# Performance work log

Hardware: AMD Instinct MI355X
Metric: run time of the kernel (lower is better)

## Reference

```python
import jax, jax.numpy as jnp
import numpy as np

B, N, D, NS, ITERS = 64, 4096, 256, 8, 3
EPS_ATTN = 1e-5   # module eps (added to attn)
EPS_LN = 1e-5     # torch LayerNorm default eps


def layer_norm(x, g, b):
    m = jnp.mean(x, axis=-1, keepdims=True)
    v = jnp.mean((x - m) ** 2, axis=-1, keepdims=True)
    return (x - m) / jnp.sqrt(v + EPS_LN) * g + b


def setup_inputs() -> dict:
    key = jax.random.key(0)
    ks = jax.random.split(key, 16)
    s = 0.02
    return {
        "inputs": jax.random.normal(ks[0], (B, N, D), jnp.float32),
        "slots_init": jax.random.normal(ks[1], (1, NS, D), jnp.float32),
        "Wq": jax.random.normal(ks[2], (D, D), jnp.float32) * s,
        "Wk": jax.random.normal(ks[3], (D, D), jnp.float32) * s,
        "Wv": jax.random.normal(ks[4], (D, D), jnp.float32) * s,
        "W_ih": jax.random.normal(ks[5], (3 * D, D), jnp.float32) * s,
        "W_hh": jax.random.normal(ks[6], (3 * D, D), jnp.float32) * s,
        "b_ih": jnp.zeros((3 * D,), jnp.float32),
        "b_hh": jnp.zeros((3 * D,), jnp.float32),
        "ln_in_g": jnp.ones((D,), jnp.float32),
        "ln_in_b": jnp.zeros((D,), jnp.float32),
        "ln_s_g": jnp.ones((D,), jnp.float32),
        "ln_s_b": jnp.zeros((D,), jnp.float32),
        "ln_m_g": jnp.ones((D,), jnp.float32),
        "ln_m_b": jnp.zeros((D,), jnp.float32),
        "W1": jax.random.normal(ks[7], (4 * D, D), jnp.float32) * s,
        "b1": jnp.zeros((4 * D,), jnp.float32),
        "W2": jax.random.normal(ks[8], (D, 4 * D), jnp.float32) * s,
        "b2": jnp.zeros((D,), jnp.float32),
    }


def gru_cell(x, h, W_ih, W_hh, b_ih, b_hh):
    # x, h: [M, D]; PyTorch GRU cell equations (gate order r, z, n)
    gi = x @ W_ih.T + b_ih
    gh = h @ W_hh.T + b_hh
    gi_r, gi_z, gi_n = jnp.split(gi, 3, axis=-1)
    gh_r, gh_z, gh_n = jnp.split(gh, 3, axis=-1)
    r = jax.nn.sigmoid(gi_r + gh_r)
    z = jax.nn.sigmoid(gi_z + gh_z)
    n = jnp.tanh(gi_n + r * gh_n)
    return (1.0 - z) * n + z * h


def reference(inputs, slots_init, Wq, Wk, Wv, W_ih, W_hh, b_ih, b_hh,
              ln_in_g, ln_in_b, ln_s_g, ln_s_b, ln_m_g, ln_m_b,
              W1, b1, W2, b2):
    b, n, d = inputs.shape
    scale = d ** -0.5
    slots = jnp.broadcast_to(slots_init, (b, NS, d))

    x = layer_norm(inputs, ln_in_g, ln_in_b)
    k = x @ Wk.T  # [b, n, d]
    v = x @ Wv.T  # [b, n, d]

    for _ in range(ITERS):
        slots_prev = slots
        s_n = layer_norm(slots, ln_s_g, ln_s_b)
        q = s_n @ Wq.T  # [b, ns, d]
        dots = jnp.einsum('bid,bjd->bij', q, k) * scale  # [b, ns, n]
        attn = jax.nn.softmax(dots, axis=1) + EPS_ATTN   # softmax over slots
        attn = attn / jnp.mean(attn, axis=-1, keepdims=True)
        updates = jnp.einsum('bjd,bij->bid', v, attn)     # [b, ns, d]
        h = gru_cell(updates.reshape(-1, d), slots_prev.reshape(-1, d),
                     W_ih, W_hh, b_ih, b_hh)
        slots = h.reshape(b, NS, d)
        # residual MLP with pre-norm
        y = layer_norm(slots, ln_m_g, ln_m_b)
        y = jax.nn.leaky_relu(y @ W1.T + b1, negative_slope=0.01)
        slots = slots + (y @ W2.T + b2)
    return slots
```

## Files before the change

kernel.cpp:

```cpp
#include <hip/hip_runtime.h>
#include <hip/hip_fp16.h>
#include <hip/hip_bf16.h>


#define BB 64
#define NN 4096
#define DD 256
#define NSL 8
#define NITER 3

__device__ __forceinline__ float wredsum(float v){
#pragma unroll
  for(int m=32;m;m>>=1) v += __shfl_xor(v, m, 64);
  return v;
}
__device__ __forceinline__ float2 u2f2(unsigned u){ __half2 h; __builtin_memcpy(&h,&u,4); return __half22float2(h); }
__device__ __forceinline__ float sigm(float v){ return 1.0f/(1.0f+__expf(-v)); }

union U4 { uint4 u; __half2 h[4]; };

__global__ __launch_bounds__(256) void k_prep(
    const float* __restrict__ Whh, const float* __restrict__ W1,
    const float* __restrict__ W2,  const float* __restrict__ sinit,
    __half* __restrict__ Wg, __half* __restrict__ W1t, __half* __restrict__ W2t,
    float* __restrict__ slots){
  for(int idx=blockIdx.x*256+threadIdx.x; idx<851968; idx+=gridDim.x*256){
    if(idx<196608){ int col=idx>>8, c=idx&255; Wg[(size_t)c*1536+768+col]=__float2half(Whh[idx]); }
    else if(idx<458752){ int k=idx-196608; int col=k>>8, c=k&255; W1t[(size_t)c*1024+col]=__float2half(W1[k]); }
    else if(idx<720896){ int k=idx-458752; int col=k>>10, c=k&1023; W2t[(size_t)c*256+col]=__float2half(W2[k]); }
    else { int k=idx-720896; slots[k]=sinit[k&2047]; }
  }
}

__global__ __launch_bounds__(256) void k_WC(const float* __restrict__ Wih, const float* __restrict__ Wv,
                                            __half* __restrict__ Wg){
  int col=blockIdx.x;
  int t=threadIdx.x;
  __shared__ float wr[256];
  wr[t]=Wih[col*256+t];
  __syncthreads();
  float acc=0.f;
#pragma unroll 8
  for(int d=0;d<256;d++) acc += wr[d]*Wv[d*256+t];
  Wg[(size_t)t*1536+col]=__float2half(acc);
}

__global__ __launch_bounds__(256) void k_M(const float* __restrict__ Wq, const float* __restrict__ Wk,
                                           __half* __restrict__ M2h){
  int c = blockIdx.x, e = threadIdx.x;
  float acc = 0.f;
#pragma unroll 8
  for(int d=0; d<256; d++) acc += Wq[d*256+e]*Wk[d*256+c];
  M2h[c*256+e] = __float2half(acc * 0.0625f);
}

__global__ __launch_bounds__(256) void k_ln_x(const float* __restrict__ in, const float* __restrict__ g,
                                              const float* __restrict__ bbv, __half* __restrict__ x){
  int row  = blockIdx.x*4 + (threadIdx.x>>6);
  int lane = threadIdx.x&63;
  const float4 v = ((const float4*)(in + (size_t)row*DD))[lane];
  float s  = v.x+v.y+v.z+v.w;
  float ss = v.x*v.x+v.y*v.y+v.z*v.z+v.w*v.w;
  s = wredsum(s); ss = wredsum(ss);
  float m = s*(1.0f/256.0f);
  float r = rsqrtf(ss*(1.0f/256.0f) - m*m + 1e-5f);
  float4 gv = ((const float4*)g)[lane];
  float4 bv = ((const float4*)bbv)[lane];
  float y0=(v.x-m)*r*gv.x+bv.x, y1=(v.y-m)*r*gv.y+bv.y;
  float y2=(v.z-m)*r*gv.z+bv.z, y3=(v.w-m)*r*gv.w+bv.w;
  __half2 h0=__floats2half2_rn(y0,y1), h1=__floats2half2_rn(y2,y3);
  uint2 u; __builtin_memcpy(&u.x,&h0,4); __builtin_memcpy(&u.y,&h1,4);
  ((uint2*)(x + (size_t)row*DD))[lane] = u;
}

__global__ __launch_bounds__(256) void k_pre(const float* __restrict__ slots, const float* __restrict__ g,
                                             const float* __restrict__ bbv, const __half* __restrict__ M2h,
                                             float* __restrict__ qs){
  int row = blockIdx.x;
  int t = threadIdx.x;
  __shared__ __align__(16) float sn[256];
  __shared__ float red[8];
  float v = slots[row*256 + t];
  float s = wredsum(v), ss = wredsum(v*v);
  int wid=t>>6, lane=t&63;
  if(lane==0){ red[wid]=s; red[4+wid]=ss; }
  __syncthreads();
  float S  = red[0]+red[1]+red[2]+red[3];
  float SS = red[4]+red[5]+red[6]+red[7];
  float m = S*(1.0f/256.0f);
  float r = rsqrtf(SS*(1.0f/256.0f) - m*m + 1e-5f);
  sn[t] = (v-m)*r*g[t]+bbv[t];
  __syncthreads();
  const uint4* w4 = (const uint4*)(M2h + (size_t)t*256);
  float acc=0.f;
#pragma unroll 4
  for(int kk=0;kk<32;kk++){
    U4 w; w.u=w4[kk];
#pragma unroll
    for(int q=0;q<4;q++){
      float2 f=__half22float2(w.h[q]);
      acc += sn[kk*8+2*q]*f.x + sn[kk*8+2*q+1]*f.y;
    }
  }
  qs[row*256+t]=acc;
}

__global__ __launch_bounds__(256) void k_att(const __half* __restrict__ x, const float* __restrict__ qs,
                                             float* __restrict__ pagg){
  int b = blockIdx.x>>4;
  int t = threadIdx.x;
  size_t j = (size_t)blockIdx.x*256 + t;
  __shared__ __align__(16) float qt[256][8];
  __shared__ __align__(16) float wl[256][8];
  __shared__ __align__(16) float aggl[4][2048];
  __shared__ float wsl[4][8];
  const float* qb = qs + b*2048;
  for(int e=t;e<2048;e+=256) qt[e&255][e>>8]=qb[e];
  __syncthreads();
  const uint4* xr = (const uint4*)(x + j*DD);
  float pd[8]={0,0,0,0,0,0,0,0};
#pragma unroll 2
  for(int ch=0; ch<32; ch++){
    uint4 u = xr[ch];
    float2 f0=u2f2(u.x), f1=u2f2(u.y), f2=u2f2(u.z), f3=u2f2(u.w);
    float xv[8]={f0.x,f0.y,f1.x,f1.y,f2.x,f2.y,f3.x,f3.y};
    int c0=ch*8;
#pragma unroll
    for(int cc=0;cc<8;cc++){
      const float4* qp=(const float4*)&qt[c0+cc][0];
      float4 qa=qp[0], qc=qp[1];
      float xvv=xv[cc];
      pd[0]+=qa.x*xvv; pd[1]+=qa.y*xvv; pd[2]+=qa.z*xvv; pd[3]+=qa.w*xvv;
      pd[4]+=qc.x*xvv; pd[5]+=qc.y*xvv; pd[6]+=qc.z*xvv; pd[7]+=qc.w*xvv;
    }
  }
  float mx=pd[0];
#pragma unroll
  for(int i=1;i<8;i++) mx=fmaxf(mx,pd[i]);
  float ev[8]; float ssum=0.f;
#pragma unroll
  for(int i=0;i<8;i++){ ev[i]=__expf(pd[i]-mx); ssum+=ev[i]; }
  float inv=1.0f/ssum;
#pragma unroll
  for(int i=0;i<8;i++) wl[t][i]=ev[i]*inv+1e-5f;
  __syncthreads();
  int wid=t>>6, lane=t&63;
  float acc[8][4];
#pragma unroll
  for(int i=0;i<8;i++){ acc[i][0]=0;acc[i][1]=0;acc[i][2]=0;acc[i][3]=0; }
  float ws[8]={0,0,0,0,0,0,0,0};
  for(int r=0;r<64;r++){
    int jl = wid*64 + r;
    uint2 u = ((const uint2*)(x + ((size_t)blockIdx.x*256 + jl)*DD))[lane];
    float2 f01=u2f2(u.x), f23=u2f2(u.y);
    const float4* wp=(const float4*)&wl[jl][0];
    float4 wa=wp[0], wb_=wp[1];
    float wv[8]={wa.x,wa.y,wa.z,wa.w,wb_.x,wb_.y,wb_.z,wb_.w};
    float xv[4]={f01.x,f01.y,f23.x,f23.y};
#pragma unroll
    for(int i=0;i<8;i++){
      acc[i][0]+=wv[i]*xv[0]; acc[i][1]+=wv[i]*xv[1];
      acc[i][2]+=wv[i]*xv[2]; acc[i][3]+=wv[i]*xv[3];
      ws[i]+=wv[i];
    }
  }
#pragma unroll
  for(int i=0;i<8;i++){
    float4 st={acc[i][0],acc[i][1],acc[i][2],acc[i][3]};
    *((float4*)&aggl[wid][i*256 + lane*4])=st;
  }
  if(lane==0){
#pragma unroll
    for(int i=0;i<8;i++) wsl[wid][i]=ws[i];
  }
  __syncthreads();
  float* pb = pagg + (size_t)blockIdx.x*2064;
  for(int e=t;e<2048;e+=256) pb[e]=aggl[0][e]+aggl[1][e]+aggl[2][e]+aggl[3][e];
  if(t<8) pb[2048+t]=wsl[0][t]+wsl[1][t]+wsl[2][t]+wsl[3][t];
}

__global__ __launch_bounds__(512) void t_gates2(
    const float* __restrict__ pagg, const float* __restrict__ slots_in,
    const __half* __restrict__ Wg, const float* __restrict__ bih, const float* __restrict__ bhh,
    const float* __restrict__ lm_g, const float* __restrict__ lm_b,
    float* __restrict__ hb, __half* __restrict__ ysh){
  int row0=blockIdx.x*2;
  int b=row0>>3, i0=row0&7;
  int t=threadIdx.x;
  int r=t>>8, c=t&255;
  __shared__ float AS[4][256];
  __shared__ __align__(16) float gl[2][1536];
  __shared__ float fac[2];
  __shared__ float redS[2][4], redQ[2][4];
  const float* pb = pagg + (size_t)b*16*2064;
  {
    float s=0.f;
#pragma unroll
    for(int ch=0;ch<16;ch++) s += pb[ch*2064 + (i0+r)*256 + c];
    AS[r][c]=s;
    AS[2+r][c]=slots_in[(size_t)(row0+r)*256+c];
  }
  if(t<2){
    float s=0.f;
#pragma unroll
    for(int ch=0;ch<16;ch++) s += pb[ch*2064 + 2048 + i0 + t];
    fac[t]=4096.0f/s;
  }
  __syncthreads();
  AS[r][c] *= fac[r];
  __syncthreads();
  if(t<384){
    int c0=t*4;
    bool ih = c0<768;
    const float* X0 = ih? AS[0] : AS[2];
    const float* X1 = ih? AS[1] : AS[3];
    const __half* wb = Wg + c0;
    float a00=0,a01=0,a02=0,a03=0, a10=0,a11=0,a12=0,a13=0;
#pragma unroll 8
    for(int k=0;k<256;k++){
      uint2 u = *(const uint2*)(wb + (size_t)k*1536);
      float2 f0=u2f2(u.x), f1=u2f2(u.y);
      float x0=X0[k], x1=X1[k];
      a00+=x0*f0.x; a01+=x0*f0.y; a02+=x0*f1.x; a03+=x0*f1.y;
      a10+=x1*f0.x; a11+=x1*f0.y; a12+=x1*f1.x; a13+=x1*f1.y;
    }
    const float* bb = ih? bih : bhh;
    int bc = ih? c0 : c0-768;
    float4 bv=*(const float4*)&bb[bc];
    gl[0][c0]=a00+bv.x; gl[0][c0+1]=a01+bv.y; gl[0][c0+2]=a02+bv.z; gl[0][c0+3]=a03+bv.w;
    gl[1][c0]=a10+bv.x; gl[1][c0+1]=a11+bv.y; gl[1][c0+2]=a12+bv.z; gl[1][c0+3]=a13+bv.w;
  }
  __syncthreads();
  {
    float gir=gl[r][c], giz=gl[r][256+c], gin=gl[r][512+c];
    float ghr=gl[r][768+c], ghz=gl[r][1024+c], ghn=gl[r][1280+c];
    float hp=AS[2+r][c];
    float rr=sigm(gir+ghr), z=sigm(giz+ghz);
    float n=tanhf(gin+rr*ghn);
    float hv=(1.0f-z)*n+z*hp;
    hb[(size_t)(row0+r)*256+c]=hv;
    float s=wredsum(hv), ss=wredsum(hv*hv);
    if((t&63)==0){ redS[r][(t>>6)&3]=s; redQ[r][(t>>6)&3]=ss; }
    __syncthreads();
    float S_=redS[r][0]+redS[r][1]+redS[r][2]+redS[r][3];
    float SS=redQ[r][0]+redQ[r][1]+redQ[r][2]+redQ[r][3];
    float m=S_*(1.0f/256.0f);
    float rs=rsqrtf(SS*(1.0f/256.0f)-m*m+1e-5f);
    ysh[(size_t)(row0+r)*256+c]=__float2half((hv-m)*rs*lm_g[c]+lm_b[c]);
  }
}

__global__ __launch_bounds__(512) void t_mlp(
    const float* __restrict__ hb, const __half* __restrict__ ysg,
    const __half* __restrict__ W1t, const float* __restrict__ b1,
    const __half* __restrict__ W2t, const float* __restrict__ b2,
    const float* __restrict__ ls_g, const float* __restrict__ ls_b,
    const __half* __restrict__ M2h,
    float* __restrict__ dst, float* __restrict__ qs, int last){
  int row0=blockIdx.x*2;
  int t=threadIdx.x;
  int r=t>>8, c=t&255;
  __shared__ float ys[2][256];
  __shared__ __align__(16) float pz[2][2][1024];
  __shared__ __align__(16) float z1[2][1024];
  __shared__ float pm[2][4][256];
  __shared__ float redS[2][4], redQ[2][4];
  ys[r][c]=__half2float(ysg[(size_t)(row0+r)*256+c]);
  __syncthreads();
  {
    int c0=c*4;
    const __half* wb = W1t + (size_t)r*128*1024 + c0;
    float a00=0,a01=0,a02=0,a03=0, a10=0,a11=0,a12=0,a13=0;
#pragma unroll 8
    for(int k=0;k<128;k++){
      uint2 u=*(const uint2*)(wb + (size_t)k*1024);
      float2 f0=u2f2(u.x), f1=u2f2(u.y);
      float x0=ys[0][r*128+k], x1=ys[1][r*128+k];
      a00+=x0*f0.x; a01+=x0*f0.y; a02+=x0*f1.x; a03+=x0*f1.y;
      a10+=x1*f0.x; a11+=x1*f0.y; a12+=x1*f1.x; a13+=x1*f1.y;
    }
    pz[r][0][c0]=a00; pz[r][0][c0+1]=a01; pz[r][0][c0+2]=a02; pz[r][0][c0+3]=a03;
    pz[r][1][c0]=a10; pz[r][1][c0+1]=a11; pz[r][1][c0+2]=a12; pz[r][1][c0+3]=a13;
  }
  __syncthreads();
  for(int idx=t; idx<2048; idx+=512){
    int rr2=idx>>10, cc=idx&1023;
    float v=pz[0][rr2][cc]+pz[1][rr2][cc]+b1[cc];
    z1[rr2][cc]= v>0.f? v : 0.01f*v;
  }
  __syncthreads();
  if(t<256){
    int ks4=t>>6, cg=t&63;
    int c0=cg*4;
    const __half* wb = W2t + (size_t)ks4*256*256 + c0;
    float a00=0,a01=0,a02=0,a03=0, a10=0,a11=0,a12=0,a13=0;
#pragma unroll 8
    for(int k=0;k<256;k++){
      uint2 u=*(const uint2*)(wb + (size_t)k*256);
      float2 f0=u2f2(u.x), f1=u2f2(u.y);
      float x0=z1[0][ks4*256+k], x1=z1[1][ks4*256+k];
      a00+=x0*f0.x; a01+=x0*f0.y; a02+=x0*f1.x; a03+=x0*f1.y;
      a10+=x1*f0.x; a11+=x1*f0.y; a12+=x1*f1.x; a13+=x1*f1.y;
    }
    pm[0][ks4][c0]=a00; pm[0][ks4][c0+1]=a01; pm[0][ks4][c0+2]=a02; pm[0][ks4][c0+3]=a03;
    pm[1][ks4][c0]=a10; pm[1][ks4][c0+1]=a11; pm[1][ks4][c0+2]=a12; pm[1][ks4][c0+3]=a13;
  }
  __syncthreads();
  float s = hb[(size_t)(row0+r)*256+c] + pm[r][0][c]+pm[r][1][c]+pm[r][2][c]+pm[r][3][c] + b2[c];
  dst[(size_t)(row0+r)*256+c]=s;
  if(last) return;
  float su=wredsum(s), sq=wredsum(s*s);
  if((t&63)==0){ redS[r][(t>>6)&3]=su; redQ[r][(t>>6)&3]=sq; }
  __syncthreads();
  float S_=redS[r][0]+redS[r][1]+redS[r][2]+redS[r][3];
  float SS=redQ[r][0]+redQ[r][1]+redQ[r][2]+redQ[r][3];
  float m=S_*(1.0f/256.0f);
  float rs=rsqrtf(SS*(1.0f/256.0f)-m*m+1e-5f);
  ys[r][c]=(s-m)*rs*ls_g[c]+ls_b[c];
  __syncthreads();
  {
    const uint4* m4=(const uint4*)(M2h+(size_t)c*256);
    float acc=0.f;
#pragma unroll 4
    for(int kk=0;kk<32;kk++){
      U4 w; w.u=m4[kk];
#pragma unroll
      for(int q=0;q<4;q++){
        float2 f=__half22float2(w.h[q]);
        acc += ys[r][kk*8+2*q]*f.x + ys[r][kk*8+2*q+1]*f.y;
      }
    }
    qs[(size_t)(row0+r)*256+c]=acc;
  }
}

extern "C" void kernel_launch(void* const* d_in, const int* in_sizes, int n_in,
                              void* d_out, int out_size, void* d_ws, size_t ws_size,
                              hipStream_t stream){
  const float* inputs=(const float*)d_in[0];
  const float* sinit =(const float*)d_in[1];
  const float* Wq =(const float*)d_in[2];
  const float* Wk =(const float*)d_in[3];
  const float* Wv =(const float*)d_in[4];
  const float* Wih=(const float*)d_in[5];
  const float* Whh=(const float*)d_in[6];
  const float* bih=(const float*)d_in[7];
  const float* bhh=(const float*)d_in[8];
  const float* lin_g=(const float*)d_in[9];
  const float* lin_b=(const float*)d_in[10];
  const float* ls_g=(const float*)d_in[11];
  const float* ls_b=(const float*)d_in[12];
  const float* lm_g=(const float*)d_in[13];
  const float* lm_b=(const float*)d_in[14];
  const float* W1=(const float*)d_in[15];
  const float* b1=(const float*)d_in[16];
  const float* W2=(const float*)d_in[17];
  const float* b2=(const float*)d_in[18];

  char* w=(char*)d_ws;
  __half* x    =(__half*)w; w += (size_t)BB*NN*DD*2;
  float* qs    =(float*)w;  w += 512*256*4;
  float* slots =(float*)w;  w += 512*256*4;
  float* pagg  =(float*)w;  w += (size_t)1024*2064*4;
  __half* M2h  =(__half*)w; w += 256*256*2;
  __half* Wg   =(__half*)w; w += 256*1536*2;
  __half* W1t  =(__half*)w; w += 256*1024*2;
  __half* W2t  =(__half*)w; w += 1024*256*2;
  float* hb    =(float*)w;  w += 512*256*4;
  __half* ysh  =(__half*)w; w += 512*256*2;

  hipLaunchKernelGGL(k_prep, dim3(1664), dim3(256), 0, stream,
                     Whh, W1, W2, sinit, Wg, W1t, W2t, slots);
  hipLaunchKernelGGL(k_WC,   dim3(768),  dim3(256), 0, stream, Wih, Wv, Wg);
  hipLaunchKernelGGL(k_M,    dim3(256),  dim3(256), 0, stream, Wq, Wk, M2h);
  hipLaunchKernelGGL(k_ln_x, dim3(65536),dim3(256), 0, stream, inputs, lin_g, lin_b, x);
  hipLaunchKernelGGL(k_pre,  dim3(512),  dim3(256), 0, stream, slots, ls_g, ls_b, M2h, qs);
  for(int it=0; it<NITER; ++it){
    int last = (it==NITER-1);
    float* dst = last ? (float*)d_out : slots;
    hipLaunchKernelGGL(k_att,    dim3(1024), dim3(256), 0, stream, x, qs, pagg);
    hipLaunchKernelGGL(t_gates2, dim3(256),  dim3(512), 0, stream, pagg, slots, Wg, bih, bhh,
                       lm_g, lm_b, hb, ysh);
    hipLaunchKernelGGL(t_mlp,    dim3(256),  dim3(512), 0, stream, hb, ysh, W1t, b1, W2t, b2,
                       ls_g, ls_b, M2h, dst, qs, last);
  }
}
```

Before: 462.2 us.

## Tile small-slot GEMMs through LDS, atomically reduce attention partials, merge prep kernels

Merges the three weight-prep kernels into one launch that also zeroes per-iteration accumulation buffers and writes a transposed copy of the Wq·Wk product. The attention kernel now reduces its partial aggregates with global atomics into per-iteration buffers, replacing the 16-way partial-buffer reduction in the gate kernel. The GRU-gate and MLP kernels now process 4 slot rows per block, staging fp16 weight tiles in shared memory, so each weight load is reused across more rows and block count halves. The intermediate post-LayerNorm activations are kept in fp32 instead of fp16. In exchange there are many more __syncthreads, fewer blocks in flight, and atomic contention in k_att.

```diff
diff --git a/kernel.cpp b/kernel.cpp
--- a/kernel.cpp
+++ b/kernel.cpp
@@ -19,39 +19,87 @@
 
 union U4 { uint4 u; __half2 h[4]; };
 
-__global__ __launch_bounds__(256) void k_prep(
+#define TG_STAGE(WSRC, LDW, C0) do{ \
+  _Pragma("unroll") \
+  for(int q=0;q<8;q++){ \
+    int u_=q*512+t; int kk_=u_>>4, cb_=u_&15; \
+    *(uint4*)&Wst[kk_][cb_*8] = *(const uint4*)((WSRC) + (size_t)kk_*(LDW) + (C0) + cb_*8); \
+  } \
+}while(0)
+
+#define TG_COMPUTE(APTR, ASTR) do{ \
+  float acc_[4][4]={{0,0,0,0},{0,0,0,0},{0,0,0,0},{0,0,0,0}}; \
+  _Pragma("unroll") \
+  for(int g_=0;g_<4;g_++){ \
+    int kb_=ks*16+g_*4; \
+    float av_[4][4]; \
+    _Pragma("unroll") \
+    for(int r_=0;r_<4;r_++){ \
+      float4 a_=*(const float4*)((APTR) + r_*(ASTR) + kb_); \
+      av_[r_][0]=a_.x; av_[r_][1]=a_.y; av_[r_][2]=a_.z; av_[r_][3]=a_.w; \
+    } \
+    _Pragma("unroll") \
+    for(int k2_=0;k2_<4;k2_++){ \
+      uint2 wv_=*(const uint2*)&Wst[kb_+k2_][c4*4]; \
+      float2 wa_=u2f2(wv_.x), wb_=u2f2(wv_.y); \
+      _Pragma("unroll") \
+      for(int r_=0;r_<4;r_++){ \
+        acc_[r_][0]+=av_[r_][k2_]*wa_.x; acc_[r_][1]+=av_[r_][k2_]*wa_.y; \
+        acc_[r_][2]+=av_[r_][k2_]*wb_.x; acc_[r_][3]+=av_[r_][k2_]*wb_.y; \
+      } \
+    } \
+  } \
+  _Pragma("unroll") \
+  for(int r_=0;r_<4;r_++){ \
+    _Pragma("unroll") \
+    for(int j_=0;j_<4;j_++) acc_[r_][j_] += __shfl_xor(acc_[r_][j_], 32, 64); \
+  } \
+  if(lane<32){ \
+    _Pragma("unroll") \
+    for(int r_=0;r_<4;r_++){ \
+      float4 v_={acc_[r_][0],acc_[r_][1],acc_[r_][2],acc_[r_][3]}; \
+      *(float4*)&pp[wid][r_][c4*4]=v_; \
+    } \
+  } \
+}while(0)
+
+__global__ __launch_bounds__(256) void kp_all(
     const float* __restrict__ Whh, const float* __restrict__ W1,
     const float* __restrict__ W2,  const float* __restrict__ sinit,
+    const float* __restrict__ Wih, const float* __restrict__ Wv,
+    const float* __restrict__ Wq,  const float* __restrict__ Wk,
     __half* __restrict__ Wg, __half* __restrict__ W1t, __half* __restrict__ W2t,
-    float* __restrict__ slots){
-  for(int idx=blockIdx.x*256+threadIdx.x; idx<851968; idx+=gridDim.x*256){
-    if(idx<196608){ int col=idx>>8, c=idx&255; Wg[(size_t)c*1536+768+col]=__float2half(Whh[idx]); }
-    else if(idx<458752){ int k=idx-196608; int col=k>>8, c=k&255; W1t[(size_t)c*1024+col]=__float2half(W1[k]); }
-    else if(idx<720896){ int k=idx-458752; int col=k>>10, c=k&1023; W2t[(size_t)c*256+col]=__float2half(W2[k]); }
-    else { int k=idx-720896; slots[k]=sinit[k&2047]; }
-  }
-}
-
-__global__ __launch_bounds__(256) void k_WC(const float* __restrict__ Wih, const float* __restrict__ Wv,
-                                            __half* __restrict__ Wg){
-  int col=blockIdx.x;
-  int t=threadIdx.x;
-  __shared__ float wr[256];
-  wr[t]=Wih[col*256+t];
-  __syncthreads();
-  float acc=0.f;
+    float* __restrict__ slots, __half* __restrict__ M2h, __half* __restrict__ M2k,
+    float* __restrict__ zbuf){
+  int bid=blockIdx.x, t=threadIdx.x;
+  if(bid<1664){
+    for(int idx=bid*256+t; idx<851968; idx+=1664*256){
+      if(idx<196608){ int col=idx>>8, c=idx&255; Wg[(size_t)c*1536+768+col]=__float2half(Whh[idx]); }
+      else if(idx<458752){ int k=idx-196608; int col=k>>8, c=k&255; W1t[(size_t)c*1024+col]=__float2half(W1[k]); }
+      else if(idx<720896){ int k=idx-458752; int col=k>>10, c=k&1023; W2t[(size_t)c*256+col]=__float2half(W2[k]); }
+      else { int k=idx-720896; slots[k]=sinit[k&2047]; }
+    }
+  } else if(bid<2432){
+    int col=bid-1664;
+    __shared__ float wr[256];
+    wr[t]=Wih[col*256+t];
+    __syncthreads();
+    float acc=0.f;
 #pragma unroll 8
-  for(int d=0;d<256;d++) acc += wr[d]*Wv[d*256+t];
-  Wg[(size_t)t*1536+col]=__float2half(acc);
-}
-
-__global__ __launch_bounds__(256) void k_M(const float* __restrict__ Wq, const float* __restrict__ Wk,
-                                           __half* __restrict__ M2h){
-  int c = blockIdx.x, e = threadIdx.x;
-  float acc = 0.f;
+    for(int d=0;d<256;d++) acc += wr[d]*Wv[d*256+t];
+    Wg[(size_t)t*1536+col]=__float2half(acc);
+  } else if(bid<2688){
+    int c=bid-2432;
+    float acc=0.f;
 #pragma unroll 8
-  for(int d=0; d<256; d++) acc += Wq[d*256+e]*Wk[d*256+c];
-  M2h[c*256+e] = __float2half(acc * 0.0625f);
+    for(int d=0;d<256;d++) acc += Wq[d*256+t]*Wk[d*256+c];
+    __half hv=__float2half(acc*0.0625f);
+    M2h[(size_t)c*256+t]=hv;
+    M2k[(size_t)t*256+c]=hv;
+  } else {
+    int idx=(bid-2688)*256+t;
+    if(idx<394752) zbuf[idx]=0.f;
+  }
 }
 
 __global__ __launch_bounds__(256) void k_ln_x(const float* __restrict__ in, const float* __restrict__ g,
@@ -106,7 +154,7 @@
 }
 
 __global__ __launch_bounds__(256) void k_att(const __half* __restrict__ x, const float* __restrict__ qs,
-                                             float* __restrict__ pagg){
+                                             float* __restrict__ aggF, float* __restrict__ wsumF){
   int b = blockIdx.x>>4;
   int t = threadIdx.x;
   size_t j = (size_t)blockIdx.x*256 + t;
@@ -174,163 +222,158 @@
     for(int i=0;i<8;i++) wsl[wid][i]=ws[i];
   }
   __syncthreads();
-  float* pb = pagg + (size_t)blockIdx.x*2064;
-  for(int e=t;e<2048;e+=256) pb[e]=aggl[0][e]+aggl[1][e]+aggl[2][e]+aggl[3][e];
-  if(t<8) pb[2048+t]=wsl[0][t]+wsl[1][t]+wsl[2][t]+wsl[3][t];
-}
-
-__global__ __launch_bounds__(512) void t_gates2(
-    const float* __restrict__ pagg, const float* __restrict__ slots_in,
-    const __half* __restrict__ Wg, const float* __restrict__ bih, const float* __restrict__ bhh,
+  float* ab = aggF + (size_t)b*2048;
+  for(int e=t;e<2048;e+=256)
+    atomicAdd(&ab[e], aggl[0][e]+aggl[1][e]+aggl[2][e]+aggl[3][e]);
+  if(t<8) atomicAdd(&wsumF[b*8+t], wsl[0][t]+wsl[1][t]+wsl[2][t]+wsl[3][t]);
+}
+
+__global__ __launch_bounds__(512) void t_g2(
+    const float* __restrict__ aggF, const float* __restrict__ wsumF,
+    const float* __restrict__ slots_in, const __half* __restrict__ Wg,
+    const float* __restrict__ bih, const float* __restrict__ bhh,
     const float* __restrict__ lm_g, const float* __restrict__ lm_b,
-    float* __restrict__ hb, __half* __restrict__ ysh){
-  int row0=blockIdx.x*2;
-  int b=row0>>3, i0=row0&7;
-  int t=threadIdx.x;
-  int r=t>>8, c=t&255;
-  __shared__ float AS[4][256];
-  __shared__ __align__(16) float gl[2][1536];
-  __shared__ float fac[2];
-  __shared__ float redS[2][4], redQ[2][4];
-  const float* pb = pagg + (size_t)b*16*2064;
-  {
-    float s=0.f;
-#pragma unroll
-    for(int ch=0;ch<16;ch++) s += pb[ch*2064 + (i0+r)*256 + c];
-    AS[r][c]=s;
-    AS[2+r][c]=slots_in[(size_t)(row0+r)*256+c];
-  }
-  if(t<2){
-    float s=0.f;
-#pragma unroll
-    for(int ch=0;ch<16;ch++) s += pb[ch*2064 + 2048 + i0 + t];
-    fac[t]=4096.0f/s;
-  }
-  __syncthreads();
-  AS[r][c] *= fac[r];
-  __syncthreads();
-  if(t<384){
-    int c0=t*4;
-    bool ih = c0<768;
-    const float* X0 = ih? AS[0] : AS[2];
-    const float* X1 = ih? AS[1] : AS[3];
-    const __half* wb = Wg + c0;
-    float a00=0,a01=0,a02=0,a03=0, a10=0,a11=0,a12=0,a13=0;
-#pragma unroll 8
-    for(int k=0;k<256;k++){
-      uint2 u = *(const uint2*)(wb + (size_t)k*1536);
-      float2 f0=u2f2(u.x), f1=u2f2(u.y);
-      float x0=X0[k], x1=X1[k];
-      a00+=x0*f0.x; a01+=x0*f0.y; a02+=x0*f1.x; a03+=x0*f1.y;
-      a10+=x1*f0.x; a11+=x1*f0.y; a12+=x1*f1.x; a13+=x1*f1.y;
-    }
-    const float* bb = ih? bih : bhh;
-    int bc = ih? c0 : c0-768;
-    float4 bv=*(const float4*)&bb[bc];
-    gl[0][c0]=a00+bv.x; gl[0][c0+1]=a01+bv.y; gl[0][c0+2]=a02+bv.z; gl[0][c0+3]=a03+bv.w;
-    gl[1][c0]=a10+bv.x; gl[1][c0+1]=a11+bv.y; gl[1][c0+2]=a12+bv.z; gl[1][c0+3]=a13+bv.w;
-  }
-  __syncthreads();
-  {
+    float* __restrict__ hb, float* __restrict__ ysf){
+  int r0=blockIdx.x*4;
+  int t=threadIdx.x, lane=t&63, wid=t>>6;
+  int c4=t&31, ks=t>>5;
+  __shared__ __align__(16) float Aih[4][256], Ahh[4][256];
+  __shared__ __align__(16) __half Wst[256][128];
+  __shared__ __align__(16) float pp[8][4][128];
+  __shared__ __align__(16) float gl[4][1536];
+  __shared__ float redS[4][4], redQ[4][4];
+  for(int u=t;u<1024;u+=512){
+    int r=u>>8, c=u&255;
+    Aih[r][c]=aggF[(size_t)(r0+r)*256+c]*(4096.0f/wsumF[r0+r]);
+    Ahh[r][c]=slots_in[(size_t)(r0+r)*256+c];
+  }
+  __syncthreads();
+  for(int ch=0; ch<12; ch++){
+    TG_STAGE(Wg, 1536, ch*128);
+    __syncthreads();
+    const float* A = (ch<6)? &Aih[0][0] : &Ahh[0][0];
+    TG_COMPUTE(A, 256);
+    __syncthreads();
+    {
+      int r=t>>7, c=t&127, col=ch*128+c;
+      float s=0.f;
+#pragma unroll
+      for(int w2=0;w2<8;w2++) s+=pp[w2][r][c];
+      gl[r][col]=s + (col<768? bih[col] : bhh[col-768]);
+    }
+    __syncthreads();
+  }
+#pragma unroll
+  for(int p=0;p<2;p++){
+    int r=(t>>8)+p*2, c=t&255;
     float gir=gl[r][c], giz=gl[r][256+c], gin=gl[r][512+c];
     float ghr=gl[r][768+c], ghz=gl[r][1024+c], ghn=gl[r][1280+c];
-    float hp=AS[2+r][c];
+    float hp=Ahh[r][c];
     float rr=sigm(gir+ghr), z=sigm(giz+ghz);
     float n=tanhf(gin+rr*ghn);
     float hv=(1.0f-z)*n+z*hp;
-    hb[(size_t)(row0+r)*256+c]=hv;
+    hb[(size_t)(r0+r)*256+c]=hv;
+    gl[r][c]=hv;
     float s=wredsum(hv), ss=wredsum(hv*hv);
-    if((t&63)==0){ redS[r][(t>>6)&3]=s; redQ[r][(t>>6)&3]=ss; }
-    __syncthreads();
-    float S_=redS[r][0]+redS[r][1]+redS[r][2]+redS[r][3];
+    if(lane==0){ redS[r][wid&3]=s; redQ[r][wid&3]=ss; }
+  }
+  __syncthreads();
+#pragma unroll
+  for(int p=0;p<2;p++){
+    int r=(t>>8)+p*2, c=t&255;
+    float S =redS[r][0]+redS[r][1]+redS[r][2]+redS[r][3];
     float SS=redQ[r][0]+redQ[r][1]+redQ[r][2]+redQ[r][3];
-    float m=S_*(1.0f/256.0f);
+    float m=S*(1.0f/256.0f);
     float rs=rsqrtf(SS*(1.0f/256.0f)-m*m+1e-5f);
-    ysh[(size_t)(row0+r)*256+c]=__float2half((hv-m)*rs*lm_g[c]+lm_b[c]);
-  }
-}
-
-__global__ __launch_bounds__(512) void t_mlp(
-    const float* __restrict__ hb, const __half* __restrict__ ysg,
+    ysf[(size_t)(r0+r)*256+c]=(gl[r][c]-m)*rs*lm_g[c]+lm_b[c];
+  }
+}
+
+__global__ __launch_bounds__(512) void t_m2(
+    const float* __restrict__ hb, const float* __restrict__ ysf,
     const __half* __restrict__ W1t, const float* __restrict__ b1,
     const __half* __restrict__ W2t, const float* __restrict__ b2,
     const float* __restrict__ ls_g, const float* __restrict__ ls_b,
-    const __half* __restrict__ M2h,
+    const __half* __restrict__ M2k,
     float* __restrict__ dst, float* __restrict__ qs, int last){
-  int row0=blockIdx.x*2;
-  int t=threadIdx.x;
-  int r=t>>8, c=t&255;
-  __shared__ float ys[2][256];
-  __shared__ __align__(16) float pz[2][2][1024];
-  __shared__ __align__(16) float z1[2][1024];
-  __shared__ float pm[2][4][256];
-  __shared__ float redS[2][4], redQ[2][4];
-  ys[r][c]=__half2float(ysg[(size_t)(row0+r)*256+c]);
-  __syncthreads();
-  {
-    int c0=c*4;
-    const __half* wb = W1t + (size_t)r*128*1024 + c0;
-    float a00=0,a01=0,a02=0,a03=0, a10=0,a11=0,a12=0,a13=0;
-#pragma unroll 8
-    for(int k=0;k<128;k++){
-      uint2 u=*(const uint2*)(wb + (size_t)k*1024);
-      float2 f0=u2f2(u.x), f1=u2f2(u.y);
-      float x0=ys[0][r*128+k], x1=ys[1][r*128+k];
-      a00+=x0*f0.x; a01+=x0*f0.y; a02+=x0*f1.x; a03+=x0*f1.y;
-      a10+=x1*f0.x; a11+=x1*f0.y; a12+=x1*f1.x; a13+=x1*f1.y;
-    }
-    pz[r][0][c0]=a00; pz[r][0][c0+1]=a01; pz[r][0][c0+2]=a02; pz[r][0][c0+3]=a03;
-    pz[r][1][c0]=a10; pz[r][1][c0+1]=a11; pz[r][1][c0+2]=a12; pz[r][1][c0+3]=a13;
-  }
-  __syncthreads();
-  for(int idx=t; idx<2048; idx+=512){
-    int rr2=idx>>10, cc=idx&1023;
-    float v=pz[0][rr2][cc]+pz[1][rr2][cc]+b1[cc];
-    z1[rr2][cc]= v>0.f? v : 0.01f*v;
-  }
-  __syncthreads();
-  if(t<256){
-    int ks4=t>>6, cg=t&63;
-    int c0=cg*4;
-    const __half* wb = W2t + (size_t)ks4*256*256 + c0;
-    float a00=0,a01=0,a02=0,a03=0, a10=0,a11=0,a12=0,a13=0;
-#pragma unroll 8
-    for(int k=0;k<256;k++){
-      uint2 u=*(const uint2*)(wb + (size_t)k*256);
-      float2 f0=u2f2(u.x), f1=u2f2(u.y);
-      float x0=z1[0][ks4*256+k], x1=z1[1][ks4*256+k];
-      a00+=x0*f0.x; a01+=x0*f0.y; a02+=x0*f1.x; a03+=x0*f1.y;
-      a10+=x1*f0.x; a11+=x1*f0.y; a12+=x1*f1.x; a13+=x1*f1.y;
-    }
-    pm[0][ks4][c0]=a00; pm[0][ks4][c0+1]=a01; pm[0][ks4][c0+2]=a02; pm[0][ks4][c0+3]=a03;
-    pm[1][ks4][c0]=a10; pm[1][ks4][c0+1]=a11; pm[1][ks4][c0+2]=a12; pm[1][ks4][c0+3]=a13;
-  }
-  __syncthreads();
-  float s = hb[(size_t)(row0+r)*256+c] + pm[r][0][c]+pm[r][1][c]+pm[r][2][c]+pm[r][3][c] + b2[c];
-  dst[(size_t)(row0+r)*256+c]=s;
+  int r0=blockIdx.x*4;
+  int t=threadIdx.x, lane=t&63, wid=t>>6;
+  int c4=t&31, ks=t>>5;
+  __shared__ __align__(16) float ysl[4][256];
+  __shared__ __align__(16) __half Wst[256][128];
+  __shared__ __align__(16) float pp[8][4][128];
+  __shared__ __align__(16) float z1[4][1024];
+  __shared__ __align__(16) float osum[4][256];
+  __shared__ float redS[4][4], redQ[4][4];
+  for(int u=t;u<1024;u+=512){ int r=u>>8,c=u&255; ysl[r][c]=ysf[(size_t)(r0+r)*256+c]; }
+  __syncthreads();
+  for(int ch=0;ch<8;ch++){
+    TG_STAGE(W1t, 1024, ch*128);
+    __syncthreads();
+    TG_COMPUTE(&ysl[0][0], 256);
+    __syncthreads();
+    {
+      int r=t>>7, c=t&127, col=ch*128+c;
+      float s=0.f;
+#pragma unroll
+      for(int w2=0;w2<8;w2++) s+=pp[w2][r][c];
+      s += b1[col];
+      z1[r][col] = s>0.f? s : 0.01f*s;
+    }
+    __syncthreads();
+  }
+  for(int kc=0;kc<4;kc++){
+    for(int cc=0;cc<2;cc++){
+      TG_STAGE(W2t + (size_t)kc*256*256, 256, cc*128);
+      __syncthreads();
+      TG_COMPUTE(&z1[0][kc*256], 1024);
+      __syncthreads();
+      {
+        int r=t>>7, c=t&127;
+        float s=0.f;
+#pragma unroll
+        for(int w2=0;w2<8;w2++) s+=pp[w2][r][c];
+        if(kc==0) osum[r][cc*128+c]=s; else osum[r][cc*128+c]+=s;
+      }
+      __syncthreads();
+    }
+  }
+#pragma unroll
+  for(int p=0;p<2;p++){
+    int r=(t>>8)+p*2, c=t&255;
+    float sv = hb[(size_t)(r0+r)*256+c] + osum[r][c] + b2[c];
+    dst[(size_t)(r0+r)*256+c]=sv;
+    osum[r][c]=sv;
+    if(!last){
+      float s=wredsum(sv), ss=wredsum(sv*sv);
+      if(lane==0){ redS[r][wid&3]=s; redQ[r][wid&3]=ss; }
+    }
+  }
   if(last) return;
-  float su=wredsum(s), sq=wredsum(s*s);
-  if((t&63)==0){ redS[r][(t>>6)&3]=su; redQ[r][(t>>6)&3]=sq; }
-  __syncthreads();
-  float S_=redS[r][0]+redS[r][1]+redS[r][2]+redS[r][3];
-  float SS=redQ[r][0]+redQ[r][1]+redQ[r][2]+redQ[r][3];
-  float m=S_*(1.0f/256.0f);
-  float rs=rsqrtf(SS*(1.0f/256.0f)-m*m+1e-5f);
-  ys[r][c]=(s-m)*rs*ls_g[c]+ls_b[c];
-  __syncthreads();
-  {
-    const uint4* m4=(const uint4*)(M2h+(size_t)c*256);
-    float acc=0.f;
-#pragma unroll 4
-    for(int kk=0;kk<32;kk++){
-      U4 w; w.u=m4[kk];
-#pragma unroll
-      for(int q=0;q<4;q++){
-        float2 f=__half22float2(w.h[q]);
-        acc += ys[r][kk*8+2*q]*f.x + ys[r][kk*8+2*q+1]*f.y;
-      }
-    }
-    qs[(size_t)(row0+r)*256+c]=acc;
+  __syncthreads();
+#pragma unroll
+  for(int p=0;p<2;p++){
+    int r=(t>>8)+p*2, c=t&255;
+    float S =redS[r][0]+redS[r][1]+redS[r][2]+redS[r][3];
+    float SS=redQ[r][0]+redQ[r][1]+redQ[r][2]+redQ[r][3];
+    float m=S*(1.0f/256.0f);
+    float rs=rsqrtf(SS*(1.0f/256.0f)-m*m+1e-5f);
+    ysl[r][c]=(osum[r][c]-m)*rs*ls_g[c]+ls_b[c];
+  }
+  __syncthreads();
+  for(int cc=0;cc<2;cc++){
+    TG_STAGE(M2k, 256, cc*128);
+    __syncthreads();
+    TG_COMPUTE(&ysl[0][0], 256);
+    __syncthreads();
+    {
+      int r=t>>7, c=t&127;
+      float s=0.f;
+#pragma unroll
+      for(int w2=0;w2<8;w2++) s+=pp[w2][r][c];
+      qs[(size_t)(r0+r)*256 + cc*128 + c]=s;
+    }
+    __syncthreads();
   }
 }
 
@@ -361,27 +404,30 @@
   __half* x    =(__half*)w; w += (size_t)BB*NN*DD*2;
   float* qs    =(float*)w;  w += 512*256*4;
   float* slots =(float*)w;  w += 512*256*4;
-  float* pagg  =(float*)w;  w += (size_t)1024*2064*4;
   __half* M2h  =(__half*)w; w += 256*256*2;
+  __half* M2k  =(__half*)w; w += 256*256*2;
   __half* Wg   =(__half*)w; w += 256*1536*2;
   __half* W1t  =(__half*)w; w += 256*1024*2;
   __half* W2t  =(__half*)w; w += 1024*256*2;
   float* hb    =(float*)w;  w += 512*256*4;
-  __half* ysh  =(__half*)w; w += 512*256*2;
-
-  hipLaunchKernelGGL(k_prep, dim3(1664), dim3(256), 0, stream,
-                     Whh, W1, W2, sinit, Wg, W1t, W2t, slots);
-  hipLaunchKernelGGL(k_WC,   dim3(768),  dim3(256), 0, stream, Wih, Wv, Wg);
-  hipLaunchKernelGGL(k_M,    dim3(256),  dim3(256), 0, stream, Wq, Wk, M2h);
+  float* ysf   =(float*)w;  w += 512*256*4;
+  float* aggZ  =(float*)w;  w += (size_t)(3*512*256 + 3*512)*4;
+
+  float* aggF[3]; float* wsumF[3];
+  for(int i=0;i<3;i++){ aggF[i]=aggZ + (size_t)i*512*256; wsumF[i]=aggZ + (size_t)3*512*256 + (size_t)i*512; }
+
+  hipLaunchKernelGGL(kp_all, dim3(4230), dim3(256), 0, stream,
+                     Whh, W1, W2, sinit, Wih, Wv, Wq, Wk,
+                     Wg, W1t, W2t, slots, M2h, M2k, aggZ);
   hipLaunchKernelGGL(k_ln_x, dim3(65536),dim3(256), 0, stream, inputs, lin_g, lin_b, x);
   hipLaunchKernelGGL(k_pre,  dim3(512),  dim3(256), 0, stream, slots, ls_g, ls_b, M2h, qs);
   for(int it=0; it<NITER; ++it){
     int last = (it==NITER-1);
     float* dst = last ? (float*)d_out : slots;
-    hipLaunchKernelGGL(k_att,    dim3(1024), dim3(256), 0, stream, x, qs, pagg);
-    hipLaunchKernelGGL(t_gates2, dim3(256),  dim3(512), 0, stream, pagg, slots, Wg, bih, bhh,
-                       lm_g, lm_b, hb, ysh);
-    hipLaunchKernelGGL(t_mlp,    dim3(256),  dim3(512), 0, stream, hb, ysh, W1t, b1, W2t, b2,
-                       ls_g, ls_b, M2h, dst, qs, last);
-  }
-}
+    hipLaunchKernelGGL(k_att, dim3(1024), dim3(256), 0, stream, x, qs, aggF[it], wsumF[it]);
+    hipLaunchKernelGGL(t_g2,  dim3(128),  dim3(512), 0, stream, aggF[it], wsumF[it], slots, Wg,
+                       bih, bhh, lm_g, lm_b, hb, ysf);
+    hipLaunchKernelGGL(t_m2,  dim3(128),  dim3(512), 0, stream, hb, ysf, W1t, b1, W2t, b2,
+                       ls_g, ls_b, M2k, dst, qs, last);
+  }
+}
```

Result: slower. 544.2 us (+17.7%).
